# Optimization experiments

Hardware: AMD Instinct MI355X
Metric: run time of the kernel (lower is better)

## Reference

```python
import jax, jax.numpy as jnp
import numpy as np

HEADS = 8
RADIUS = 50
EPS = 1e-5


def conv1d(x, w, b, stride, pad):
    # x: [B, Cin, T], w: [Cout, Cin, K] (torch OIH layout)
    y = jax.lax.conv_general_dilated(x, w, (stride,), [(pad, pad)],
                                     dimension_numbers=("NCH", "OIH", "NCH"))
    return y + b[None, :, None]


def mm1x1(x, w, b):
    # pointwise Conv1d: w [Cout, Cin]
    return jnp.einsum("oc,bct->bot", w, x) + b[None, :, None]


def lstm_layer(xT, Wih, Whh, bih, bhh):
    # xT: [T, B, Cin]; torch gate order i, f, g, o
    B = xT.shape[1]
    Hh = Whh.shape[1]
    h0 = jnp.zeros((B, Hh), xT.dtype)

    def step(carry, xt):
        h, c = carry
        g = xt @ Wih.T + h @ Whh.T + bih + bhh
        i, f, gg, o = jnp.split(g, 4, axis=-1)
        c = jax.nn.sigmoid(f) * c + jax.nn.sigmoid(i) * jnp.tanh(gg)
        h = jax.nn.sigmoid(o) * jnp.tanh(c)
        return (h, c), h

    _, ys = jax.lax.scan(step, (h0, h0), xT)
    return ys


def attention(x, q_w, q_b, k_w, k_b, c_w, c_b, rel_emb, fc_w, fc_b, bn_g, bn_b, attn_scale):
    B, C, L = x.shape
    D = C // HEADS
    split = lambda y: y.reshape(B, HEADS, D, L)
    q = split(mm1x1(x, q_w, q_b))
    k = split(mm1x1(x, k_w, k_b))
    cnt = split(mm1x1(x, c_w, c_b))
    dots = jnp.einsum("bhct,bhcs->bhts", q, k)  # no 1/sqrt(d): faithful to source
    steps = jnp.arange(L)
    rel = steps[:, None] - steps[None, :]                       # [L, L]
    embs = rel_emb[RADIUS + jnp.clip(rel, -RADIUS, RADIUS)]     # [L, L, D]
    dots = dots + 0.3 * jnp.einsum("bhct,tsc->bhts", q, embs)
    dots = jnp.where((jnp.abs(rel) <= RADIUS)[None, None], dots, -jnp.inf)
    w = jax.nn.softmax(dots, axis=-1)
    out = jnp.einsum("bhts,bhcs->bhct", w, cnt) + 0.3 * jnp.einsum("bhts,tsc->bhct", w, embs)
    out = out.reshape(B, C, L)
    out = mm1x1(out, fc_w, fc_b)
    # BatchNorm1d, training-mode statistics over (batch, time)
    mu = out.mean(axis=(0, 2), keepdims=True)
    var = ((out - mu) ** 2).mean(axis=(0, 2), keepdims=True)
    out = (out - mu) * jax.lax.rsqrt(var + EPS) * bn_g[None, :, None] + bn_b[None, :, None]
    return jax.nn.relu(out) * attn_scale[None, :, None]


def forward(meg, conv1_w, conv1_b, conv2_w, conv2_b, subj_emb,
            W_ih0, W_hh0, b_ih0, b_hh0, W_ih1, W_hh1, b_ih1, b_hh1,
            q_w, q_b, k_w, k_b, c_w, c_b, rel_emb, fc_w, fc_b, bn_g, bn_b,
            attn_scale, out_w, out_b, subjects):
    # ConvSequence encoder: two strided convs, LeakyReLU(0.0) == ReLU
    x = jax.nn.relu(conv1d(meg, conv1_w, conv1_b, 2, 2))
    x = jax.nn.relu(conv1d(x, conv2_w, conv2_b, 2, 2))          # [B, 512, L]
    B, _, L = x.shape
    emb = subj_emb[subjects]                                    # ScaledEmbedding, scale=1.0
    x = jnp.concatenate([x, jnp.broadcast_to(emb[:, :, None], (B, emb.shape[1], L))], axis=1)
    xT = x.transpose(2, 0, 1)                                   # [L, B, 576]
    xT = lstm_layer(xT, W_ih0, W_hh0, b_ih0, b_hh0)
    xT = lstm_layer(xT, W_ih1, W_hh1, b_ih1, b_hh1)
    x = xT.transpose(1, 2, 0)                                   # [B, 512, L]
    x = x + attention(x, q_w, q_b, k_w, k_b, c_w, c_b, rel_emb, fc_w, fc_b, bn_g, bn_b, attn_scale)
    return mm1x1(x, out_w, out_b)                               # [B, 128, L]


def setup_inputs() -> dict:
    key = jax.random.key(0)
    ks = iter(jax.random.split(key, 40))
    nk = lambda: next(ks)
    r = lambda shape, s=0.05: jax.random.normal(nk(), shape, jnp.float32) * s
    # relative-position embedding with the cumsum/sqrt init from the source
    rel = jax.random.normal(nk(), (2 * RADIUS + 1, 64), jnp.float32) * 0.05
    rel = jnp.cumsum(rel, axis=0) / jnp.sqrt(jnp.arange(1, 2 * RADIUS + 2, dtype=jnp.float32))[:, None]
    return dict(
        meg=jax.random.normal(nk(), (8, 273, 2048), jnp.float32),
        conv1_w=r((512, 273, 4)), conv1_b=r((512,)),
        conv2_w=r((512, 512, 4)), conv2_b=r((512,)),
        subj_emb=r((200, 64), 0.1),
        W_ih0=r((2048, 576)), W_hh0=r((2048, 512)), b_ih0=r((2048,)), b_hh0=r((2048,)),
        W_ih1=r((2048, 512)), W_hh1=r((2048, 512)), b_ih1=r((2048,)), b_hh1=r((2048,)),
        q_w=r((512, 512)), q_b=r((512,)),
        k_w=r((512, 512)), k_b=r((512,)),
        c_w=r((512, 512)), c_b=r((512,)),
        rel_emb=rel,
        fc_w=r((512, 512)), fc_b=r((512,)),
        bn_g=jnp.ones((512,), jnp.float32), bn_b=jnp.zeros((512,), jnp.float32),
        attn_scale=jnp.full((512,), 0.1, jnp.float32),
        out_w=r((128, 512)), out_b=r((128,)),
        subjects=jax.random.randint(nk(), (8,), 0, 200),
    )


def reference(meg, conv1_w, conv1_b, conv2_w, conv2_b, subj_emb,
              W_ih0, W_hh0, b_ih0, b_hh0, W_ih1, W_hh1, b_ih1, b_hh1,
              q_w, q_b, k_w, k_b, c_w, c_b, rel_emb, fc_w, fc_b, bn_g, bn_b,
              attn_scale, out_w, out_b, subjects):
    return forward(meg, conv1_w, conv1_b, conv2_w, conv2_b, subj_emb,
                   W_ih0, W_hh0, b_ih0, b_hh0, W_ih1, W_hh1, b_ih1, b_hh1,
                   q_w, q_b, k_w, k_b, c_w, c_b, rel_emb, fc_w, fc_b, bn_g, bn_b,
                   attn_scale, out_w, out_b, subjects)
```

## Files before the change

kernel.cpp:

```cpp
#include <hip/hip_runtime.h>
#include <cstdint>
#include <cmath>

typedef unsigned short u16;
typedef unsigned int u32;
typedef __attribute__((ext_vector_type(8))) short bf16x8;
typedef __attribute__((ext_vector_type(4))) float f32x4;

#define B_    8
#define T_IN  2048
#define CIN1  273
#define L1_   1025
#define L_    513
#define C_    512
#define CE_   576
#define M1_   (B_*L1_)
#define M_    (B_*L_)
#define K1_   (CIN1*4)
#define H_    8
#define D_    64
#define R_    50

__device__ __forceinline__ u32 f2bf_rne(float f) {
    u32 x = __float_as_uint(f);
    return (x + 0x7fffu + ((x >> 16) & 1u)) >> 16;
}

__device__ __forceinline__ u32 a_pair(const void* A, int m, int k, int lda, int amode, int Ksz) {
    if (amode == 2) {
        if (k >= K1_) return 0;
        int b = m / L1_, t = m - b * L1_;
        int ci = k >> 2, kk = k & 3;
        int it = 2 * t - 2 + kk;
        const float* mg = (const float*)A + ((size_t)(b * CIN1 + ci)) * T_IN;
        u32 lo = ((unsigned)it < (unsigned)T_IN)       ? f2bf_rne(mg[it])     : 0;
        u32 hi = ((unsigned)(it + 1) < (unsigned)T_IN) ? f2bf_rne(mg[it + 1]) : 0;
        return lo | (hi << 16);
    } else if (amode == 5) {
        int b = m / L_, t = m - b * L_;
        int kk = k >> 9, ci = k & 511;
        int it = 2 * t - 2 + kk;
        if ((unsigned)it >= (unsigned)L1_) return 0;
        return *(const u32*)((const u16*)A + ((size_t)(b * L1_ + it)) * 512 + ci);
    } else {
        return *(const u32*)((const u16*)A + (size_t)m * lda + k);
    }
}

__global__ __launch_bounds__(256) void gemm_kernel(
    const void* __restrict__ Aptr, const u32* __restrict__ Bp,
    const float* __restrict__ bias1, const float* __restrict__ bias2,
    float* __restrict__ Cf, u16* __restrict__ Cb,
    int Msz, int Nsz, int Ksz, int lda, int ldc, int amode, int cmode, int relu)
{
    __shared__ u16 As[64][40];
    __shared__ u16 Bs[64][40];

    int tid = threadIdx.x;
    int m0 = blockIdx.x * 64, n0 = blockIdx.y * 64;
    int wv = tid >> 6, lane = tid & 63;
    int lm = lane & 15, quad = lane >> 4;
    int kp = tid & 15, rw = tid >> 4;
    int Kh = Ksz >> 1;

    f32x4 acc[4];
#pragma unroll
    for (int nt = 0; nt < 4; ++nt)
#pragma unroll
        for (int r = 0; r < 4; ++r) acc[nt][r] = 0.f;

    for (int k0 = 0; k0 < Ksz; k0 += 32) {
        int pidx = (k0 >> 1) + kp;
#pragma unroll
        for (int i = 0; i < 4; ++i) {
            int row = rw + 16 * i;
            int k = k0 + 2 * kp;
            int m = m0 + row;
            u32 aw = 0;
            if (m < Msz && k < Ksz) aw = a_pair(Aptr, m, k, lda, amode, Ksz);
            *(u32*)&As[row][2 * kp] = aw;
            u32 bw = 0;
            if (pidx < Kh) bw = Bp[(size_t)(n0 + row) * Kh + pidx];
            *(u32*)&Bs[row][2 * kp] = bw;
        }
        __syncthreads();

        bf16x8 af = *(const bf16x8*)&As[wv * 16 + lm][quad * 8];
#pragma unroll
        for (int nt = 0; nt < 4; ++nt) {
            bf16x8 bf = *(const bf16x8*)&Bs[nt * 16 + lm][quad * 8];
            acc[nt] = __builtin_amdgcn_mfma_f32_16x16x32_bf16(af, bf, acc[nt], 0, 0, 0);
        }
        __syncthreads();
    }

#pragma unroll
    for (int nt = 0; nt < 4; ++nt) {
#pragma unroll
        for (int r = 0; r < 4; ++r) {
            int m = m0 + wv * 16 + quad * 4 + r;
            if (m >= Msz) continue;
            int n = n0 + nt * 16 + lm;
            float v = acc[nt][r] + bias1[n] + (bias2 ? bias2[n] : 0.f);
            if (relu) v = fmaxf(v, 0.f);
            if (cmode == 0) {
                Cf[(size_t)m * ldc + n] = v;
            } else if (cmode == 1) {
                int b = m / L_, t = m - b * L_;
                Cf[((size_t)(b * 128 + n)) * L_ + t] = v;
            } else if (cmode == 2) {
                int b = m / L_, t = m - b * L_;
                Cf[((size_t)(t * 8 + b)) * ldc + n] = v;
            } else {
                Cb[(size_t)m * ldc + n] = (u16)f2bf_rne(v);
            }
        }
    }
}

__global__ __launch_bounds__(256) void gemm_qkv(
    const u16* __restrict__ h1b,
    const u32* __restrict__ qwp, const u32* __restrict__ kwp, const u32* __restrict__ cwp,
    const float* __restrict__ qb, const float* __restrict__ kb, const float* __restrict__ cb,
    float* __restrict__ qo, float* __restrict__ ko, float* __restrict__ co)
{
    __shared__ u16 As[64][40];
    __shared__ u16 Bs[64][40];

    int tid = threadIdx.x;
    int which = blockIdx.y >> 3;
    int m0 = blockIdx.x * 64, n0 = (blockIdx.y & 7) * 64;
    const u32* Bp = which == 0 ? qwp : (which == 1 ? kwp : cwp);
    const float* bias = which == 0 ? qb : (which == 1 ? kb : cb);
    float* Cf = which == 0 ? qo : (which == 1 ? ko : co);

    int wv = tid >> 6, lane = tid & 63;
    int lm = lane & 15, quad = lane >> 4;
    int kp = tid & 15, rw = tid >> 4;

    f32x4 acc[4];
#pragma unroll
    for (int nt = 0; nt < 4; ++nt)
#pragma unroll
        for (int r = 0; r < 4; ++r) acc[nt][r] = 0.f;

    for (int k0 = 0; k0 < 512; k0 += 32) {
#pragma unroll
        for (int i = 0; i < 4; ++i) {
            int row = rw + 16 * i;
            int k = k0 + 2 * kp;
            int m = m0 + row;
            u32 aw = 0;
            if (m < M_) {
                int b = m / L_, t = m - b * L_;
                aw = *(const u32*)(h1b + ((size_t)(t * 8 + b)) * 512 + k);
            }
            *(u32*)&As[row][2 * kp] = aw;
            *(u32*)&Bs[row][2 * kp] = Bp[(size_t)(n0 + row) * 256 + (k0 >> 1) + kp];
        }
        __syncthreads();

        bf16x8 af = *(const bf16x8*)&As[wv * 16 + lm][quad * 8];
#pragma unroll
        for (int nt = 0; nt < 4; ++nt) {
            bf16x8 bf = *(const bf16x8*)&Bs[nt * 16 + lm][quad * 8];
            acc[nt] = __builtin_amdgcn_mfma_f32_16x16x32_bf16(af, bf, acc[nt], 0, 0, 0);
        }
        __syncthreads();
    }

#pragma unroll
    for (int nt = 0; nt < 4; ++nt) {
#pragma unroll
        for (int r = 0; r < 4; ++r) {
            int m = m0 + wv * 16 + quad * 4 + r;
            if (m >= M_) continue;
            int n = n0 + nt * 16 + lm;
            Cf[(size_t)m * 512 + n] = acc[nt][r] + bias[n];
        }
    }
}

__global__ __launch_bounds__(256) void emb_kernel(const float* __restrict__ semb,
                                                  const int* __restrict__ subj,
                                                  u16* __restrict__ x2b)
{
    int idx = blockIdx.x * 256 + threadIdx.x;
    if (idx >= M_ * 64) return;
    int m = idx >> 6, e = idx & 63;
    int b = m / L_;
    x2b[(size_t)m * CE_ + 512 + e] = (u16)f2bf_rne(semb[subj[b] * 64 + e]);
}

__global__ __launch_bounds__(256) void pack_b(const float* __restrict__ W, u32* __restrict__ P,
                                              int N, int K)
{
    int gid = blockIdx.x * 256 + threadIdx.x;
    int Kh = K >> 1;
    if (gid >= N * Kh) return;
    int n = gid / Kh, p = gid - n * Kh;
    int k = 2 * p;
    u32 lo = f2bf_rne(W[(size_t)n * K + k]);
    u32 hi = f2bf_rne(W[(size_t)n * K + k + 1]);
    P[gid] = lo | (hi << 16);
}

__global__ __launch_bounds__(256) void pack_post(const float* __restrict__ qw,
                                                 const float* __restrict__ kw,
                                                 const float* __restrict__ cw,
                                                 const float* __restrict__ fcw,
                                                 const float* __restrict__ outw,
                                                 u32* __restrict__ P)
{
    int gid = blockIdx.x * 256 + threadIdx.x;
    if (gid >= 557056) return;
    const float* W;
    int local;
    if (gid < 524288) {
        int wsel = gid >> 17;
        W = wsel == 0 ? qw : (wsel == 1 ? kw : (wsel == 2 ? cw : fcw));
        local = gid & 131071;
    } else {
        W = outw;
        local = gid - 524288;
    }
    int n = local >> 8, p = local & 255;
    int k = 2 * p;
    u32 lo = f2bf_rne(W[(size_t)n * 512 + k]);
    u32 hi = f2bf_rne(W[(size_t)n * 512 + k + 1]);
    P[gid] = lo | (hi << 16);
}

__global__ __launch_bounds__(256) void pack_w2k(const float* __restrict__ W, u32* __restrict__ P)
{
    int gid = blockIdx.x * 256 + threadIdx.x;
    int n = gid >> 10, p = gid & 1023;
    int kk = p >> 8, ci = (2 * p) & 511;
    u32 lo = f2bf_rne(W[(size_t)n * 2048 + ci * 4 + kk]);
    u32 hi = f2bf_rne(W[(size_t)n * 2048 + ci * 4 + 4 + kk]);
    P[gid] = lo | (hi << 16);
}

__global__ __launch_bounds__(256) void pack_w3(const float* __restrict__ W0,
                                               const float* __restrict__ W1,
                                               const float* __restrict__ W2,
                                               u32* __restrict__ P)
{
    int gid3 = blockIdx.x * 256 + threadIdx.x;
    int src = gid3 >> 19;
    int gid = gid3 & 524287;
    const float* W = src == 0 ? W0 : (src == 1 ? W1 : W2);
    int r = gid & 1, lane = (gid >> 1) & 63, i2 = (gid >> 7) & 1;
    int g = (gid >> 8) & 3, j = gid >> 10;
    int row = g * 512 + j;
    int c0 = 4 * (lane + 64 * i2) + 2 * r;
    u32 lo = f2bf_rne(W[(size_t)row * 512 + c0]);
    u32 hi = f2bf_rne(W[(size_t)row * 512 + c0 + 1]);
    P[gid3] = lo | (hi << 16);
}

__global__ __launch_bounds__(256, 1) void lstm_step_fused(
    const float* __restrict__ pre0,
    const u32* __restrict__ P0,
    const u32* __restrict__ P1,
    const u32* __restrict__ P2,
    const float* __restrict__ bih1,
    const float* __restrict__ bhh1,
    float* __restrict__ h0seq,
    float* __restrict__ h1seq,
    u16* __restrict__ h1b,
    float* __restrict__ c0st, float* __restrict__ c1st,
    int t)
{
    int layer = blockIdx.x >> 7;
    int blk = blockIdx.x & 127;
    if (layer == 0 && t >= L_) return;
    if (layer == 1 && t == 0) return;
    int tt = layer ? (t - 1) : t;

    int tid = threadIdx.x;
    int l  = tid & 63;
    int rg = tid >> 6;
    int j = blk * 4 + rg;

    __shared__ float4 hA4[1024];
    __shared__ float4 hB4[1024];
    __shared__ float part[4 * 8 * 33];
    __shared__ float gates[4 * 33];

    const u32* wA = (layer ? P2 : P0) + (size_t)j * 1024;
    uint2 wra[8], wrb[8];
#pragma unroll
    for (int i2 = 0; i2 < 2; ++i2)
#pragma unroll
        for (int g = 0; g < 4; ++g)
            wra[i2 * 4 + g] = *(const uint2*)&wA[(g * 2 + i2) * 128 + l * 2];
    if (layer) {
        const u32* wB = P1 + (size_t)j * 1024;
#pragma unroll
        for (int i2 = 0; i2 < 2; ++i2)
#pragma unroll
            for (int g = 0; g < 4; ++g)
                wrb[i2 * 4 + g] = *(const uint2*)&wB[(g * 2 + i2) * 128 + l * 2];
    }
    float mypre = 0.f;
    if (tid < 128) {
        int fw = tid >> 5, fb = tid & 7;
        int grow = ((tid & 31) >> 3) * 512 + blk * 4 + fw;
        mypre = layer ? (bih1[grow] + bhh1[grow])
                      : pre0[((size_t)(tt * 8 + fb)) * 2048 + grow];
    }

    if (tt == 0) {
#pragma unroll
        for (int i = 0; i < 4; ++i)
            hA4[tid + 256 * i] = make_float4(0.f, 0.f, 0.f, 0.f);
    } else {
        const float4* src = (const float4*)((layer ? h1seq : h0seq) + (size_t)(tt - 1) * 4096);
#pragma unroll
        for (int i = 0; i < 4; ++i)
            hA4[tid + 256 * i] = src[tid + 256 * i];
    }
    if (layer) {
        const float4* src = (const float4*)(h0seq + (size_t)tt * 4096);
#pragma unroll
        for (int i = 0; i < 4; ++i)
            hB4[tid + 256 * i] = src[tid + 256 * i];
    }
    __syncthreads();

    float acc[4][8];
#pragma unroll
    for (int g = 0; g < 4; ++g)
#pragma unroll
        for (int b = 0; b < 8; ++b) acc[g][b] = 0.f;

#pragma unroll
    for (int i2 = 0; i2 < 2; ++i2) {
        int cq = l + 64 * i2;
        float4 hv[8];
#pragma unroll
        for (int b = 0; b < 8; ++b) hv[b] = hA4[b * 128 + cq];
#pragma unroll
        for (int g = 0; g < 4; ++g) {
            uint2 ww = wra[i2 * 4 + g];
            float w0 = __uint_as_float(ww.x << 16);
            float w1 = __uint_as_float(ww.x & 0xffff0000u);
            float w2 = __uint_as_float(ww.y << 16);
            float w3 = __uint_as_float(ww.y & 0xffff0000u);
#pragma unroll
            for (int b = 0; b < 8; ++b)
                acc[g][b] = fmaf(w0, hv[b].x, fmaf(w1, hv[b].y,
                            fmaf(w2, hv[b].z, fmaf(w3, hv[b].w, acc[g][b]))));
        }
    }
    if (layer) {
#pragma unroll
        for (int i2 = 0; i2 < 2; ++i2) {
            int cq = l + 64 * i2;
            float4 hv[8];
#pragma unroll
            for (int b = 0; b < 8; ++b) hv[b] = hB4[b * 128 + cq];
#pragma unroll
            for (int g = 0; g < 4; ++g) {
                uint2 ww = wrb[i2 * 4 + g];
                float w0 = __uint_as_float(ww.x << 16);
                float w1 = __uint_as_float(ww.x & 0xffff0000u);
                float w2 = __uint_as_float(ww.y << 16);
                float w3 = __uint_as_float(ww.y & 0xffff0000u);
#pragma unroll
                for (int b = 0; b < 8; ++b)
                    acc[g][b] = fmaf(w0, hv[b].x, fmaf(w1, hv[b].y,
                                fmaf(w2, hv[b].z, fmaf(w3, hv[b].w, acc[g][b]))));
            }
        }
    }

#pragma unroll
    for (int m = 8; m <= 32; m <<= 1)
#pragma unroll
        for (int g = 0; g < 4; ++g)
#pragma unroll
            for (int b = 0; b < 8; ++b)
                acc[g][b] += __shfl_xor(acc[g][b], m);
    if (l < 8) {
#pragma unroll
        for (int g = 0; g < 4; ++g)
#pragma unroll
            for (int b = 0; b < 8; ++b)
                part[(rg * 8 + l) * 33 + g * 8 + b] = acc[g][b];
    }
    __syncthreads();

    if (tid < 128) {
        int w = tid >> 5, x = tid & 31;
        float s = 0.f;
#pragma unroll
        for (int p = 0; p < 8; ++p) s += part[(w * 8 + p) * 33 + x];
        gates[w * 33 + x] = s + mypre;
    }
    __syncthreads();

    if (tid < 32) {
        int w = tid >> 3, b = tid & 7;
        float gi = gates[w * 33 + 0 * 8 + b];
        float gf = gates[w * 33 + 1 * 8 + b];
        float gg = gates[w * 33 + 2 * 8 + b];
        float go = gates[w * 33 + 3 * 8 + b];
        float* cst = layer ? c1st : c0st;
        int ji = blk * 4 + w;
        int ci = b * 512 + ji;
        float cprev = (tt == 0) ? 0.f : cst[ci];
        float si = 1.f / (1.f + expf(-gi));
        float sf = 1.f / (1.f + expf(-gf));
        float so = 1.f / (1.f + expf(-go));
        float cn = sf * cprev + si * tanhf(gg);
        cst[ci] = cn;
        float hv = so * tanhf(cn);
        float* hout = layer ? h1seq : h0seq;
        hout[((size_t)tt * 8 + b) * 512 + ji] = hv;
        if (layer) h1b[((size_t)tt * 8 + b) * 512 + ji] = (u16)f2bf_rne(hv);
    }
}

__global__ __launch_bounds__(128) void attn_kernel(const float* __restrict__ q,
                                                   const float* __restrict__ k,
                                                   const float* __restrict__ cnt,
                                                   const float* __restrict__ rel,
                                                   u16* __restrict__ outb)
{
    int t = blockIdx.x, h = blockIdx.y, b = blockIdx.z;
    int s_lo = max(0, t - R_), s_hi = min(L_ - 1, t + R_);
    int W = s_hi - s_lo + 1;
    int tid = threadIdx.x;

    __shared__ float qrow[64];
    __shared__ float dots[104];
    __shared__ float red[128];

    const float* qp = q + ((size_t)(b * L_ + t) * C_ + h * D_);
    if (tid < 64) qrow[tid] = qp[tid];
    __syncthreads();

    if (tid < W) {
        int s = s_lo + tid;
        const float* kp = k + ((size_t)(b * L_ + s) * C_ + h * D_);
        const float* rp = rel + (R_ + t - s) * D_;
        float acc = 0.f;
#pragma unroll 8
        for (int d = 0; d < 64; ++d)
            acc += qrow[d] * (kp[d] + 0.3f * rp[d]);
        dots[tid] = acc;
    }
    __syncthreads();

    red[tid] = (tid < W) ? dots[tid] : -INFINITY;
    __syncthreads();
    for (int s = 64; s > 0; s >>= 1) {
        if (tid < s) red[tid] = fmaxf(red[tid], red[tid + s]);
        __syncthreads();
    }
    float mx = red[0];
    __syncthreads();
    float e = 0.f;
    if (tid < W) { e = expf(dots[tid] - mx); dots[tid] = e; }
    red[tid] = e;
    __syncthreads();
    for (int s = 64; s > 0; s >>= 1) {
        if (tid < s) red[tid] += red[tid + s];
        __syncthreads();
    }
    float inv = 1.f / red[0];
    if (tid < W) dots[tid] *= inv;
    __syncthreads();

    if (tid < 64) {
        float acc = 0.f;
        const float* cb = cnt + ((size_t)(b * L_ + s_lo) * C_ + h * D_ + tid);
        const float* rb = rel + (R_ + t - s_lo) * D_ + tid;
        for (int i = 0; i < W; ++i)
            acc += dots[i] * (cb[(size_t)i * C_] + 0.3f * rb[-i * D_]);
        outb[(size_t)(b * L_ + t) * C_ + h * D_ + tid] = (u16)f2bf_rne(acc);
    }
}

__global__ __launch_bounds__(512) void bn_sum(const float* __restrict__ fcout, float* __restrict__ stats)
{
    int c = threadIdx.x;
    float s = 0.f, ss = 0.f;
    for (int m = blockIdx.x; m < M_; m += 32) {
        float v = fcout[(size_t)m * 512 + c];
        s += v; ss += v * v;
    }
    atomicAdd(&stats[c], s);
    atomicAdd(&stats[512 + c], ss);
}

__global__ __launch_bounds__(256) void bn_apply(const float* __restrict__ fcout,
                                                const float* __restrict__ stats,
                                                const float* __restrict__ bng, const float* __restrict__ bnb,
                                                const float* __restrict__ ascl,
                                                const float* __restrict__ h1tm,
                                                u16* __restrict__ xfinb)
{
    int idx = blockIdx.x * 256 + threadIdx.x;
    if (idx >= M_ * 512) return;
    int c = idx & 511;
    int m = idx >> 9;
    int b = m / L_, t = m - b * L_;
    float mean = stats[c] * (1.f / (float)M_);
    float var = stats[512 + c] * (1.f / (float)M_) - mean * mean;
    float rs = rsqrtf(fmaxf(var, 0.f) + 1e-5f);
    float v = (fcout[idx] - mean) * rs * bng[c] + bnb[c];
    v = fmaxf(v, 0.f) * ascl[c];
    xfinb[idx] = (u16)f2bf_rne(h1tm[((size_t)(t * 8 + b)) * 512 + c] + v);
}

extern "C" void kernel_launch(void* const* d_in, const int* in_sizes, int n_in,
                              void* d_out, int out_size, void* d_ws, size_t ws_size,
                              hipStream_t stream)
{
    const float* meg  = (const float*)d_in[0];
    const float* w1   = (const float*)d_in[1];
    const float* b1   = (const float*)d_in[2];
    const float* w2   = (const float*)d_in[3];
    const float* b2   = (const float*)d_in[4];
    const float* semb = (const float*)d_in[5];
    const float* Wih0 = (const float*)d_in[6];
    const float* Whh0 = (const float*)d_in[7];
    const float* bih0 = (const float*)d_in[8];
    const float* bhh0 = (const float*)d_in[9];
    const float* Wih1 = (const float*)d_in[10];
    const float* Whh1 = (const float*)d_in[11];
    const float* bih1 = (const float*)d_in[12];
    const float* bhh1 = (const float*)d_in[13];
    const float* qw   = (const float*)d_in[14];
    const float* qb   = (const float*)d_in[15];
    const float* kw   = (const float*)d_in[16];
    const float* kb   = (const float*)d_in[17];
    const float* cw   = (const float*)d_in[18];
    const float* cbi  = (const float*)d_in[19];
    const float* rel  = (const float*)d_in[20];
    const float* fcw  = (const float*)d_in[21];
    const float* fcb  = (const float*)d_in[22];
    const float* bng  = (const float*)d_in[23];
    const float* bnb  = (const float*)d_in[24];
    const float* ascl = (const float*)d_in[25];
    const float* outw = (const float*)d_in[26];
    const float* outb = (const float*)d_in[27];
    const int* subj = (const int*)d_in[28];
    float* out = (float*)d_out;

    float* ws = (float*)d_ws;
    u16*   x1b   = (u16*)(ws + 0);
    u32*   w1p   = (u32*)(ws + 6562304);
    u32*   w2p   = (u32*)(ws + 6841856);
    u16*   x2b   = (u16*)(ws + 4198400);
    u32*   wih0p = (u32*)(ws + 14967296);
    u32*   P0    = (u32*)(ws + 0);
    u32*   P1    = (u32*)(ws + 524288);
    u32*   P2    = (u32*)(ws + 1048576);
    float* c0    = ws + 1572864;
    float* c1    = ws + 1576960;
    float* pre0  = ws + 6562304;
    float* h0    = ws + 14967296;
    float* h1    = ws + 17068544;
    u16*   h1b   = (u16*)(ws + 19169792);
    float* qb_f  = ws + 0;
    float* kb_f  = ws + 2101248;
    float* cb_f  = ws + 4202496;
    u16*   attno = (u16*)(ws + 6562304);
    float* fco   = ws + 8663552;
    float* stats = ws + 10764800;
    u32*   qwp   = (u32*)(ws + 10765824);
    u32*   kwp   = (u32*)(ws + 10896896);
    u32*   cwp   = (u32*)(ws + 11027968);
    u32*   fcwp  = (u32*)(ws + 11159040);
    u32*   outwp = (u32*)(ws + 11290112);
    u16*   xfinb = (u16*)(ws + 19169792);

    auto gemm = [&](const void* A, const u32* Bp, const float* bi1, const float* bi2,
                    float* Cf, u16* Cb, int Msz, int Nsz, int Ksz,
                    int lda, int ldc, int amode, int cmode, int relu) {
        dim3 g((Msz + 63) / 64, Nsz / 64);
        gemm_kernel<<<g, 256, 0, stream>>>(A, Bp, bi1, bi2, Cf, Cb,
                                           Msz, Nsz, Ksz, lda, ldc, amode, cmode, relu);
    };

    pack_b<<<(512 * 546 + 255) / 256, 256, 0, stream>>>(w1, w1p, 512, 1092);
    pack_w2k<<<2048, 256, 0, stream>>>(w2, w2p);

    gemm(meg, w1p, b1, nullptr, nullptr, x1b, M1_, 512, K1_, 0, 512, 2, 3, 1);
    gemm(x1b, w2p, b2, nullptr, nullptr, x2b, M_, 512, 2048, 0, CE_, 5, 3, 1);
    emb_kernel<<<(M_ * 64 + 255) / 256, 256, 0, stream>>>(semb, subj, x2b);

    pack_w3<<<6144, 256, 0, stream>>>(Whh0, Wih1, Whh1, P0);
    pack_b<<<(2048 * 288 + 255) / 256, 256, 0, stream>>>(Wih0, wih0p, 2048, 576);

    gemm(x2b, wih0p, bih0, bhh0, pre0, nullptr, M_, 2048, CE_, CE_, 2048, 6, 2, 0);

    for (int t = 0; t <= L_; ++t)
        lstm_step_fused<<<256, 256, 0, stream>>>(pre0, P0, P1, P2, bih1, bhh1,
                                                 h0, h1, h1b, c0, c1, t);

    pack_post<<<(557056 + 255) / 256, 256, 0, stream>>>(qw, kw, cw, fcw, outw, qwp);
    hipMemsetAsync(stats, 0, 1024 * sizeof(float), stream);

    gemm_qkv<<<dim3((M_ + 63) / 64, 24), 256, 0, stream>>>(h1b, qwp, kwp, cwp, qb, kb, cbi,
                                                           qb_f, kb_f, cb_f);

    attn_kernel<<<dim3(L_, H_, B_), 128, 0, stream>>>(qb_f, kb_f, cb_f, rel, attno);

    gemm(attno, fcwp, fcb, nullptr, fco, nullptr, M_, 512, 512, 512, 512, 6, 0, 0);
    bn_sum<<<32, 512, 0, stream>>>(fco, stats);
    bn_apply<<<(M_ * 512 + 255) / 256, 256, 0, stream>>>(fco, stats, bng, bnb, ascl, h1, xfinb);

    gemm(xfinb, outwp, outb, nullptr, out, nullptr, M_, 128, 512, 512, 0, 6, 1, 0);
}
```

Measured before the change: 4.314 ms.

## Replace per-step LSTM launches with one persistent kernel using flag-based sync

Replaces the 514 per-timestep kernel launches with a single persistent kernel of 256 blocks. Each block keeps its weights in registers and spins on agent-scope atomic counters until the previous step of its own layer (and, for layer 1, the matching layer-0 step) has finished. The cell state now lives in a register instead of global memory. This removes launch overhead and repeated weight reloads, but correctness depends on all 256 blocks being resident at once, otherwise the spin-waits can deadlock.

```diff
diff --git a/kernel.cpp b/kernel.cpp
--- a/kernel.cpp
+++ b/kernel.cpp
@@ -259,7 +259,7 @@
     P[gid3] = lo | (hi << 16);
 }
 
-__global__ __launch_bounds__(256, 1) void lstm_step_fused(
+__global__ __launch_bounds__(256, 1) void lstm_persist(
     const float* __restrict__ pre0,
     const u32* __restrict__ P0,
     const u32* __restrict__ P1,
@@ -269,19 +269,15 @@
     float* __restrict__ h0seq,
     float* __restrict__ h1seq,
     u16* __restrict__ h1b,
-    float* __restrict__ c0st, float* __restrict__ c1st,
-    int t)
-{
-    int layer = blockIdx.x >> 7;
-    int blk = blockIdx.x & 127;
-    if (layer == 0 && t >= L_) return;
-    if (layer == 1 && t == 0) return;
-    int tt = layer ? (t - 1) : t;
-
-    int tid = threadIdx.x;
-    int l  = tid & 63;
-    int rg = tid >> 6;
-    int j = blk * 4 + rg;
+    unsigned* __restrict__ f0,
+    unsigned* __restrict__ f1)
+{
+    const int layer = blockIdx.x >> 7;
+    const int blk = blockIdx.x & 127;
+    const int tid = threadIdx.x;
+    const int l = tid & 63;
+    const int rg = tid >> 6;
+    const int j = blk * 4 + rg;
 
     __shared__ float4 hA4[1024];
     __shared__ float4 hB4[1024];
@@ -303,67 +299,75 @@
             for (int g = 0; g < 4; ++g)
                 wrb[i2 * 4 + g] = *(const uint2*)&wB[(g * 2 + i2) * 128 + l * 2];
     }
-    float mypre = 0.f;
+
+    int fb = 0, grow = 0;
+    float bias1 = 0.f;
     if (tid < 128) {
-        int fw = tid >> 5, fb = tid & 7;
-        int grow = ((tid & 31) >> 3) * 512 + blk * 4 + fw;
-        mypre = layer ? (bih1[grow] + bhh1[grow])
-                      : pre0[((size_t)(tt * 8 + fb)) * 2048 + grow];
-    }
-
-    if (tt == 0) {
-#pragma unroll
-        for (int i = 0; i < 4; ++i)
-            hA4[tid + 256 * i] = make_float4(0.f, 0.f, 0.f, 0.f);
-    } else {
-        const float4* src = (const float4*)((layer ? h1seq : h0seq) + (size_t)(tt - 1) * 4096);
-#pragma unroll
-        for (int i = 0; i < 4; ++i)
-            hA4[tid + 256 * i] = src[tid + 256 * i];
-    }
-    if (layer) {
-        const float4* src = (const float4*)(h0seq + (size_t)tt * 4096);
-#pragma unroll
-        for (int i = 0; i < 4; ++i)
-            hB4[tid + 256 * i] = src[tid + 256 * i];
-    }
-    __syncthreads();
-
-    float acc[4][8];
-#pragma unroll
-    for (int g = 0; g < 4; ++g)
-#pragma unroll
-        for (int b = 0; b < 8; ++b) acc[g][b] = 0.f;
-
-#pragma unroll
-    for (int i2 = 0; i2 < 2; ++i2) {
-        int cq = l + 64 * i2;
-        float4 hv[8];
-#pragma unroll
-        for (int b = 0; b < 8; ++b) hv[b] = hA4[b * 128 + cq];
-#pragma unroll
-        for (int g = 0; g < 4; ++g) {
-            uint2 ww = wra[i2 * 4 + g];
-            float w0 = __uint_as_float(ww.x << 16);
-            float w1 = __uint_as_float(ww.x & 0xffff0000u);
-            float w2 = __uint_as_float(ww.y << 16);
-            float w3 = __uint_as_float(ww.y & 0xffff0000u);
-#pragma unroll
-            for (int b = 0; b < 8; ++b)
-                acc[g][b] = fmaf(w0, hv[b].x, fmaf(w1, hv[b].y,
-                            fmaf(w2, hv[b].z, fmaf(w3, hv[b].w, acc[g][b]))));
-        }
-    }
-    if (layer) {
+        int fw = tid >> 5;
+        fb = tid & 7;
+        grow = ((tid & 31) >> 3) * 512 + blk * 4 + fw;
+        if (layer) bias1 = bih1[grow] + bhh1[grow];
+    }
+
+    float creg = 0.f;
+
+    for (int t = 0; t <= L_; ++t) {
+        bool active = layer ? (t >= 1) : (t < L_);
+        if (!active) continue;
+        int tt = layer ? (t - 1) : t;
+
+        if (tid == 0) {
+            if (layer) {
+                while (__hip_atomic_load(&f0[tt], __ATOMIC_RELAXED, __HIP_MEMORY_SCOPE_AGENT) < 128u)
+                    __builtin_amdgcn_s_sleep(2);
+                if (tt > 0)
+                    while (__hip_atomic_load(&f1[tt - 1], __ATOMIC_RELAXED, __HIP_MEMORY_SCOPE_AGENT) < 128u)
+                        __builtin_amdgcn_s_sleep(2);
+            } else if (tt > 0) {
+                while (__hip_atomic_load(&f0[tt - 1], __ATOMIC_RELAXED, __HIP_MEMORY_SCOPE_AGENT) < 128u)
+                    __builtin_amdgcn_s_sleep(2);
+            }
+        }
+        __syncthreads();
+        __builtin_amdgcn_fence(__ATOMIC_ACQUIRE, "agent");
+
+        float mypre = 0.f;
+        if (tid < 128)
+            mypre = layer ? bias1 : pre0[((size_t)(tt * 8 + fb)) * 2048 + grow];
+
+        if (tt == 0) {
+#pragma unroll
+            for (int i = 0; i < 4; ++i)
+                hA4[tid + 256 * i] = make_float4(0.f, 0.f, 0.f, 0.f);
+        } else {
+            const float4* src = (const float4*)((layer ? h1seq : h0seq) + (size_t)(tt - 1) * 4096);
+#pragma unroll
+            for (int i = 0; i < 4; ++i)
+                hA4[tid + 256 * i] = src[tid + 256 * i];
+        }
+        if (layer) {
+            const float4* src = (const float4*)(h0seq + (size_t)tt * 4096);
+#pragma unroll
+            for (int i = 0; i < 4; ++i)
+                hB4[tid + 256 * i] = src[tid + 256 * i];
+        }
+        __syncthreads();
+
+        float acc[4][8];
+#pragma unroll
+        for (int g = 0; g < 4; ++g)
+#pragma unroll
+            for (int b = 0; b < 8; ++b) acc[g][b] = 0.f;
+
 #pragma unroll
         for (int i2 = 0; i2 < 2; ++i2) {
             int cq = l + 64 * i2;
             float4 hv[8];
 #pragma unroll
-            for (int b = 0; b < 8; ++b) hv[b] = hB4[b * 128 + cq];
+            for (int b = 0; b < 8; ++b) hv[b] = hA4[b * 128 + cq];
 #pragma unroll
             for (int g = 0; g < 4; ++g) {
-                uint2 ww = wrb[i2 * 4 + g];
+                uint2 ww = wra[i2 * 4 + g];
                 float w0 = __uint_as_float(ww.x << 16);
                 float w1 = __uint_as_float(ww.x & 0xffff0000u);
                 float w2 = __uint_as_float(ww.y << 16);
@@ -374,52 +378,75 @@
                                 fmaf(w2, hv[b].z, fmaf(w3, hv[b].w, acc[g][b]))));
             }
         }
-    }
-
-#pragma unroll
-    for (int m = 8; m <= 32; m <<= 1)
-#pragma unroll
-        for (int g = 0; g < 4; ++g)
-#pragma unroll
-            for (int b = 0; b < 8; ++b)
-                acc[g][b] += __shfl_xor(acc[g][b], m);
-    if (l < 8) {
-#pragma unroll
-        for (int g = 0; g < 4; ++g)
-#pragma unroll
-            for (int b = 0; b < 8; ++b)
-                part[(rg * 8 + l) * 33 + g * 8 + b] = acc[g][b];
-    }
-    __syncthreads();
-
-    if (tid < 128) {
-        int w = tid >> 5, x = tid & 31;
-        float s = 0.f;
-#pragma unroll
-        for (int p = 0; p < 8; ++p) s += part[(w * 8 + p) * 33 + x];
-        gates[w * 33 + x] = s + mypre;
-    }
-    __syncthreads();
-
-    if (tid < 32) {
-        int w = tid >> 3, b = tid & 7;
-        float gi = gates[w * 33 + 0 * 8 + b];
-        float gf = gates[w * 33 + 1 * 8 + b];
-        float gg = gates[w * 33 + 2 * 8 + b];
-        float go = gates[w * 33 + 3 * 8 + b];
-        float* cst = layer ? c1st : c0st;
-        int ji = blk * 4 + w;
-        int ci = b * 512 + ji;
-        float cprev = (tt == 0) ? 0.f : cst[ci];
-        float si = 1.f / (1.f + expf(-gi));
-        float sf = 1.f / (1.f + expf(-gf));
-        float so = 1.f / (1.f + expf(-go));
-        float cn = sf * cprev + si * tanhf(gg);
-        cst[ci] = cn;
-        float hv = so * tanhf(cn);
-        float* hout = layer ? h1seq : h0seq;
-        hout[((size_t)tt * 8 + b) * 512 + ji] = hv;
-        if (layer) h1b[((size_t)tt * 8 + b) * 512 + ji] = (u16)f2bf_rne(hv);
+        if (layer) {
+#pragma unroll
+            for (int i2 = 0; i2 < 2; ++i2) {
+                int cq = l + 64 * i2;
+                float4 hv[8];
+#pragma unroll
+                for (int b = 0; b < 8; ++b) hv[b] = hB4[b * 128 + cq];
+#pragma unroll
+                for (int g = 0; g < 4; ++g) {
+                    uint2 ww = wrb[i2 * 4 + g];
+                    float w0 = __uint_as_float(ww.x << 16);
+                    float w1 = __uint_as_float(ww.x & 0xffff0000u);
+                    float w2 = __uint_as_float(ww.y << 16);
+                    float w3 = __uint_as_float(ww.y & 0xffff0000u);
+#pragma unroll
+                    for (int b = 0; b < 8; ++b)
+                        acc[g][b] = fmaf(w0, hv[b].x, fmaf(w1, hv[b].y,
+                                    fmaf(w2, hv[b].z, fmaf(w3, hv[b].w, acc[g][b]))));
+                }
+            }
+        }
+
+#pragma unroll
+        for (int m = 8; m <= 32; m <<= 1)
+#pragma unroll
+            for (int g = 0; g < 4; ++g)
+#pragma unroll
+                for (int b = 0; b < 8; ++b)
+                    acc[g][b] += __shfl_xor(acc[g][b], m);
+        if (l < 8) {
+#pragma unroll
+            for (int g = 0; g < 4; ++g)
+#pragma unroll
+                for (int b = 0; b < 8; ++b)
+                    part[(rg * 8 + l) * 33 + g * 8 + b] = acc[g][b];
+        }
+        __syncthreads();
+
+        if (tid < 128) {
+            int w = tid >> 5, x = tid & 31;
+            float s = 0.f;
+#pragma unroll
+            for (int p = 0; p < 8; ++p) s += part[(w * 8 + p) * 33 + x];
+            gates[w * 33 + x] = s + mypre;
+        }
+        __syncthreads();
+
+        if (tid < 32) {
+            int w = tid >> 3, b = tid & 7;
+            float gi = gates[w * 33 + 0 * 8 + b];
+            float gf = gates[w * 33 + 1 * 8 + b];
+            float gg = gates[w * 33 + 2 * 8 + b];
+            float go = gates[w * 33 + 3 * 8 + b];
+            int ji = blk * 4 + w;
+            float cprev = (tt == 0) ? 0.f : creg;
+            float si = 1.f / (1.f + expf(-gi));
+            float sf = 1.f / (1.f + expf(-gf));
+            float so = 1.f / (1.f + expf(-go));
+            float cn = sf * cprev + si * tanhf(gg);
+            creg = cn;
+            float hv = so * tanhf(cn);
+            float* hout = layer ? h1seq : h0seq;
+            hout[((size_t)tt * 8 + b) * 512 + ji] = hv;
+            if (layer) h1b[((size_t)tt * 8 + b) * 512 + ji] = (u16)f2bf_rne(hv);
+        }
+        __syncthreads();
+        if (tid == 0)
+            __hip_atomic_fetch_add(layer ? &f1[tt] : &f0[tt], 1u,
+                                   __ATOMIC_RELEASE, __HIP_MEMORY_SCOPE_AGENT);
     }
 }
 
@@ -560,8 +587,7 @@
     u32*   P0    = (u32*)(ws + 0);
     u32*   P1    = (u32*)(ws + 524288);
     u32*   P2    = (u32*)(ws + 1048576);
-    float* c0    = ws + 1572864;
-    float* c1    = ws + 1576960;
+    unsigned* flg = (unsigned*)(ws + 1572864);
     float* pre0  = ws + 6562304;
     float* h0    = ws + 14967296;
     float* h1    = ws + 17068544;
@@ -599,9 +625,9 @@
 
     gemm(x2b, wih0p, bih0, bhh0, pre0, nullptr, M_, 2048, CE_, CE_, 2048, 6, 2, 0);
 
-    for (int t = 0; t <= L_; ++t)
-        lstm_step_fused<<<256, 256, 0, stream>>>(pre0, P0, P1, P2, bih1, bhh1,
-                                                 h0, h1, h1b, c0, c1, t);
+    hipMemsetAsync(flg, 0, 1028 * sizeof(unsigned), stream);
+    lstm_persist<<<dim3(256), 256, 0, stream>>>(pre0, P0, P1, P2, bih1, bhh1,
+                                                h0, h1, h1b, flg, flg + 514);
 
     pack_post<<<(557056 + 255) / 256, 256, 0, stream>>>(qw, kw, cw, fcw, outw, qwp);
     hipMemsetAsync(stats, 0, 1024 * sizeof(float), stream);
```

Result: slower. 8.751 ms (+102.9%).
